# Kernel optimization log

Measured on AMD Instinct MI355X. Metric: run time of the kernel, lower is better.

## Reference

```python
import jax, jax.numpy as jnp
import numpy as np

EPS = 1e-5  # torch LayerNorm default


def setup_inputs() -> dict:
    key = jax.random.key(0)
    ks = jax.random.split(key, 4)
    N, E, D_IN, D_OUT = 10000, 640000, 128, 128
    x = jax.random.normal(ks[0], (N, D_IN), dtype=jnp.float32)
    edge_index = jax.random.randint(ks[1], (2, E), 0, N, dtype=jnp.int64)
    edge_weight = jax.random.uniform(ks[2], (E,), dtype=jnp.float32)
    W = jax.random.normal(ks[3], (D_IN, D_OUT), dtype=jnp.float32) / np.sqrt(D_IN)
    b = jnp.zeros((D_OUT,), dtype=jnp.float32)
    gamma = jnp.ones((D_OUT,), dtype=jnp.float32)
    beta = jnp.zeros((D_OUT,), dtype=jnp.float32)
    return {"x": x, "edge_index": edge_index, "edge_weight": edge_weight,
            "W": W, "b": b, "gamma": gamma, "beta": beta}


def reference(x, edge_index, edge_weight, W, b, gamma, beta):
    N = x.shape[0]
    src, dst = edge_index[0], edge_index[1]
    # in-degree (scatter_add of ones onto dst)
    deg = jax.ops.segment_sum(jnp.ones(dst.shape[0], dtype=x.dtype), dst,
                              num_segments=N)
    deg_inv = (deg + 1.0) ** -0.5  # [N]
    # gather-scale: per-edge messages [E, D]
    msgs = x[src] * deg_inv[src][:, None] * edge_weight[:, None]
    # scatter-add aggregation back to nodes [N, D]
    agg = jax.ops.segment_sum(msgs, dst, num_segments=N)
    agg = agg * deg_inv[:, None] + x  # symmetric norm + residual
    # linear + exact gelu (torch default) ; dropout is identity at eval
    h = jax.nn.gelu(agg @ W + b, approximate=False)
    # LayerNorm over last dim
    mu = jnp.mean(h, axis=-1, keepdims=True)
    var = jnp.mean((h - mu) ** 2, axis=-1, keepdims=True)
    return (h - mu) * jax.lax.rsqrt(var + EPS) * gamma + beta
```

## Files before the change

### kernel.cpp

```cpp
#include <hip/hip_runtime.h>
#include <math.h>


#define D 128
#define NB 512
#define NBK 256
#define MAXCHUNK 2560
#define MAXB 1600
#define FPSCALE 2097152.0f
#define FPINV (1.0f / 2097152.0f)

typedef short bf16x8 __attribute__((ext_vector_type(8)));
typedef float f32x4 __attribute__((ext_vector_type(4)));

static __device__ __forceinline__ unsigned bf16bits(float v) {
    unsigned u = __float_as_uint(v);
    return (u + 0x7fffu + ((u >> 16) & 1u)) >> 16;
}
static __device__ __forceinline__ int bkt_of(int d, unsigned N) {
    return (int)(((unsigned)d * NB) / N);
}
static __device__ __forceinline__ int bkt_start(int b, unsigned N) {
    return (int)(((unsigned)b * N + NB - 1) / NB);
}

__global__ __launch_bounds__(1024) void k_scatter(const int* __restrict__ srcIdx,
                                                  const int* __restrict__ dstIdx,
                                                  const float* __restrict__ ew,
                                                  uint2* __restrict__ tmp,
                                                  int* __restrict__ rp,
                                                  int E, int chunk, unsigned N) {
    __shared__ int hist[NB];
    __shared__ int scn[NB];
    __shared__ int cur[NB];
    __shared__ int dsts[MAXCHUNK];
    __shared__ uint2 sbuf[MAXCHUNK];
    int t = threadIdx.x, bb = blockIdx.x;
    int e0 = bb * chunk;
    int e1 = e0 + chunk; if (e1 > E) e1 = E;
    int n_loc = e1 - e0; if (n_loc < 0) n_loc = 0;
    for (int i = t; i < NB; i += 1024) hist[i] = 0;
    __syncthreads();
    for (int i = t; i < n_loc; i += 1024) {
        int d = dstIdx[e0 + i];
        dsts[i] = d;
        atomicAdd(&hist[bkt_of(d, N)], 1);
    }
    __syncthreads();
    if (t < NB) scn[t] = hist[t];
    __syncthreads();
    for (int o = 1; o < NB; o <<= 1) {
        int v = 0;
        if (t < NB && t >= o) v = scn[t - o];
        __syncthreads();
        if (t < NB && t >= o) scn[t] += v;
        __syncthreads();
    }
    if (t < NB) {
        int excl = scn[t] - hist[t];
        cur[t] = excl;
        rp[bb * (NB + 1) + t] = excl;
    }
    if (t == 0) rp[bb * (NB + 1) + NB] = n_loc;
    __syncthreads();
    for (int i = t; i < n_loc; i += 1024) {
        int d = dsts[i];
        int bin = bkt_of(d, N);
        int dl = d - bkt_start(bin, N);
        int pos = atomicAdd(&cur[bin], 1);
        sbuf[pos] = make_uint2((unsigned)srcIdx[e0 + i] | ((unsigned)dl << 16),
                               __float_as_uint(ew[e0 + i]));
    }
    __syncthreads();
    for (int i = t; i < n_loc; i += 1024)
        tmp[e0 + i] = sbuf[i];
}

__global__ __launch_bounds__(256) void k_xsdeg(const float* __restrict__ x,
                                               const uint2* __restrict__ tmp,
                                               const int* __restrict__ rp,
                                               unsigned* __restrict__ xs,
                                               int chunk, unsigned N) {
    __shared__ int segoff[NBK];
    __shared__ int segsrc[NBK];
    __shared__ int h[24];
    __shared__ float dinv[24];
    int b = blockIdx.x, t = threadIdx.x;
    int start = bkt_start(b, N), end = bkt_start(b + 1, N);
    int nn = end - start;
    if (t < NBK) {
        int lo = rp[t * (NB + 1) + b];
        int hi = rp[t * (NB + 1) + b + 1];
        segoff[t] = hi - lo;
        segsrc[t] = t * chunk + lo;
    }
    if (t < 24) h[t] = 0;
    __syncthreads();
    for (int o = 1; o < NBK; o <<= 1) {
        int v = 0;
        if (t < NBK && t >= o) v = segoff[t - o];
        __syncthreads();
        if (t < NBK && t >= o) segoff[t] += v;
        __syncthreads();
    }
    int cnt = segoff[NBK - 1];
    for (int i = t; i < cnt; i += 256) {
        int lo2 = 0, hi2 = NBK - 1;
        while (lo2 < hi2) { int mid = (lo2 + hi2) >> 1; if (segoff[mid] > i) hi2 = mid; else lo2 = mid + 1; }
        int base = lo2 ? segoff[lo2 - 1] : 0;
        uint2 rec = tmp[segsrc[lo2] + (i - base)];
        atomicAdd(&h[rec.x >> 16], 1);
    }
    __syncthreads();
    if (t < nn) dinv[t] = rsqrtf((float)h[t] + 1.0f);
    __syncthreads();
    for (int i = t; i < nn * 64; i += 256) {
        int nl = i >> 6, l = i & 63;
        int node = start + nl;
        float s = dinv[nl];
        float f0 = x[node * D + l] * s;
        float f1 = x[node * D + 64 + l] * s;
        xs[node * 64 + l] = bf16bits(f0) | (bf16bits(f1) << 16);
    }
}

__global__ __launch_bounds__(512) void k_mega(
    const float* __restrict__ x, const unsigned* __restrict__ xs,
    const uint2* __restrict__ tmp, const int* __restrict__ rp,
    const float* __restrict__ W, const float* __restrict__ bias,
    const float* __restrict__ gamma, const float* __restrict__ beta,
    float* __restrict__ out, int chunk, unsigned N) {
    __shared__ unsigned short wb[16384];
    __shared__ int segoff[NBK];
    __shared__ int segsrc[NBK];
    __shared__ uint2 reg1[MAXB];
    __shared__ unsigned reg2[2176];
    __shared__ int acc[20 * 128];
    __shared__ int h[24], st[24], cur[24];
    __shared__ float dinvs[24];
    __shared__ float bias_s[128], gamma_s[128], beta_s[128];
    __shared__ float s1s[4][2], s2s[4][2];

    float* hls = (float*)reg1;
    unsigned short* absb = (unsigned short*)reg2;
    unsigned* fin = reg2;

    int b = blockIdx.x, t = threadIdx.x;
    int start = bkt_start(b, N), end = bkt_start(b + 1, N);
    int nn = end - start;
    int wv = t >> 6, l = t & 63;

    for (int idx = t; idx < D * D; idx += 512) {
        int k = idx >> 7, n = idx & 127;
        wb[((k >> 3) * 128 + n) * 8 + (k & 7)] = (unsigned short)bf16bits(W[idx]);
    }
    if (t < 128) { bias_s[t] = bias[t]; gamma_s[t] = gamma[t]; beta_s[t] = beta[t]; }
    if (t < 24) h[t] = 0;

    if (t < NBK) {
        int lo = rp[t * (NB + 1) + b];
        int hi = rp[t * (NB + 1) + b + 1];
        segoff[t] = hi - lo;
        segsrc[t] = t * chunk + lo;
    }
    __syncthreads();
    for (int o = 1; o < NBK; o <<= 1) {
        int v = 0;
        if (t < NBK && t >= o) v = segoff[t - o];
        __syncthreads();
        if (t < NBK && t >= o) segoff[t] += v;
        __syncthreads();
    }
    int cnt = segoff[NBK - 1];
    int cntc = cnt > MAXB ? MAXB : cnt;

    for (int i = t; i < cntc; i += 512) {
        int lo2 = 0, hi2 = NBK - 1;
        while (lo2 < hi2) { int mid = (lo2 + hi2) >> 1; if (segoff[mid] > i) hi2 = mid; else lo2 = mid + 1; }
        int base = lo2 ? segoff[lo2 - 1] : 0;
        uint2 rec = tmp[segsrc[lo2] + (i - base)];
        reg1[i] = rec;
        atomicAdd(&h[rec.x >> 16], 1);
    }
    for (int i = t; i < 20 * 128; i += 512) acc[i] = 0;
    __syncthreads();

    if (t == 0) {
        st[0] = 0;
        for (int d2 = 0; d2 < nn; ++d2) st[d2 + 1] = st[d2] + h[d2];
    }
    if (t < nn) dinvs[t] = rsqrtf((float)h[t] + 1.0f);
    __syncthreads();
    if (t < nn) cur[t] = st[t];
    __syncthreads();

    for (int i = t; i < cntc; i += 512) {
        uint2 rec = reg1[i];
        int dl = (int)(rec.x >> 16);
        int pos = atomicAdd(&cur[dl], 1);
        fin[pos] = (rec.x & 0xffffu) | (bf16bits(__uint_as_float(rec.y)) << 16);
    }
    __syncthreads();

    {
        int lo = (int)(((long long)cntc * wv) >> 3);
        int hi = (int)(((long long)cntc * (wv + 1)) >> 3);
        if (lo < hi) {
            int dl = 0;
            while (st[dl + 1] <= lo) ++dl;
            float a0 = 0.0f, a1 = 0.0f;
            int i = lo;
            while (i < hi) {
                if (i >= st[dl + 1]) {
                    atomicAdd(&acc[dl * 128 + l], (int)(a0 * FPSCALE));
                    atomicAdd(&acc[dl * 128 + 64 + l], (int)(a1 * FPSCALE));
                    a0 = 0.0f; a1 = 0.0f;
                    do { ++dl; } while (i >= st[dl + 1]);
                }
                int stop = st[dl + 1] < hi ? st[dl + 1] : hi;
                for (; i + 4 <= stop; i += 4) {
                    unsigned p0 = fin[i], p1 = fin[i + 1], p2 = fin[i + 2], p3 = fin[i + 3];
                    unsigned q0 = xs[(p0 & 0xffffu) * 64u + (unsigned)l];
                    unsigned q1 = xs[(p1 & 0xffffu) * 64u + (unsigned)l];
                    unsigned q2 = xs[(p2 & 0xffffu) * 64u + (unsigned)l];
                    unsigned q3 = xs[(p3 & 0xffffu) * 64u + (unsigned)l];
                    float w0 = __uint_as_float(p0 & 0xffff0000u);
                    float w1 = __uint_as_float(p1 & 0xffff0000u);
                    float w2 = __uint_as_float(p2 & 0xffff0000u);
                    float w3 = __uint_as_float(p3 & 0xffff0000u);
                    a0 = fmaf(__uint_as_float(q0 << 16), w0, a0);
                    a1 = fmaf(__uint_as_float(q0 & 0xffff0000u), w0, a1);
                    a0 = fmaf(__uint_as_float(q1 << 16), w1, a0);
                    a1 = fmaf(__uint_as_float(q1 & 0xffff0000u), w1, a1);
                    a0 = fmaf(__uint_as_float(q2 << 16), w2, a0);
                    a1 = fmaf(__uint_as_float(q2 & 0xffff0000u), w2, a1);
                    a0 = fmaf(__uint_as_float(q3 << 16), w3, a0);
                    a1 = fmaf(__uint_as_float(q3 & 0xffff0000u), w3, a1);
                }
                for (; i < stop; ++i) {
                    unsigned p = fin[i];
                    float wt = __uint_as_float(p & 0xffff0000u);
                    unsigned q = xs[(p & 0xffffu) * 64u + (unsigned)l];
                    a0 = fmaf(__uint_as_float(q << 16), wt, a0);
                    a1 = fmaf(__uint_as_float(q & 0xffff0000u), wt, a1);
                }
            }
            atomicAdd(&acc[dl * 128 + l], (int)(a0 * FPSCALE));
            atomicAdd(&acc[dl * 128 + 64 + l], (int)(a1 * FPSCALE));
        }
    }
    __syncthreads();

    for (int i = t; i < 32 * 128; i += 512) {
        int row = i >> 7, col = i & 127;
        unsigned short v = 0;
        if (row < nn) {
            float aggv = (float)acc[row * 128 + col] * FPINV * dinvs[row]
                         + x[(start + row) * D + col];
            v = (unsigned short)bf16bits(aggv);
        }
        absb[row * 136 + col] = v;
    }
    __syncthreads();

    {
        int col = l & 15, quad = l >> 4;
#pragma unroll
        for (int ti = 0; ti < 2; ++ti) {
            int tid = wv * 2 + ti;
            int mt = tid >> 3, nt = tid & 7;
            f32x4 dacc = {0.0f, 0.0f, 0.0f, 0.0f};
#pragma unroll
            for (int kk = 0; kk < 4; ++kk) {
                bf16x8 av = *(const bf16x8*)&absb[(mt * 16 + col) * 136 + kk * 32 + quad * 8];
                bf16x8 bv = *(const bf16x8*)&wb[((kk * 4 + quad) * 128 + nt * 16 + col) * 8];
                dacc = __builtin_amdgcn_mfma_f32_16x16x32_bf16(av, bv, dacc, 0, 0, 0);
            }
#pragma unroll
            for (int r = 0; r < 4; ++r) {
                int m = mt * 16 + quad * 4 + r;
                int n = nt * 16 + col;
                if (m < 20) {
                    float hh = dacc[r] + bias_s[n];
                    hh = 0.5f * hh * (1.0f + erff(hh * 0.70710678f));
                    hls[m * 129 + n] = hh;
                }
            }
        }
    }
    __syncthreads();

    {
        int g = t >> 7;
        int tt = t & 127;
        int w2 = (t >> 6) & 1;
        for (int r = 0; r < 5; ++r) {
            int dl = r * 4 + g;
            bool valid = dl < nn;
            float hh = valid ? hls[dl * 129 + tt] : 0.0f;
            float v1 = hh, v2 = hh * hh;
#pragma unroll
            for (int o = 32; o > 0; o >>= 1) {
                v1 += __shfl_xor(v1, o, 64);
                v2 += __shfl_xor(v2, o, 64);
            }
            if (l == 0) { s1s[g][w2] = v1; s2s[g][w2] = v2; }
            __syncthreads();
            float s1 = s1s[g][0] + s1s[g][1];
            float s2 = s2s[g][0] + s2s[g][1];
            float mu = s1 * (1.0f / D);
            float var = s2 * (1.0f / D) - mu * mu;
            float rinv = rsqrtf(var + 1e-5f);
            if (valid)
                out[(start + dl) * D + tt] = (hh - mu) * rinv * gamma_s[tt] + beta_s[tt];
            __syncthreads();
        }
    }
}

static inline size_t align256(size_t v) { return (v + 255) & ~(size_t)255; }

extern "C" void kernel_launch(void* const* d_in, const int* in_sizes, int n_in,
                              void* d_out, int out_size, void* d_ws, size_t ws_size,
                              hipStream_t stream) {
    const float* x     = (const float*)d_in[0];
    const int*   ei    = (const int*)d_in[1];
    const float* ew    = (const float*)d_in[2];
    const float* W     = (const float*)d_in[3];
    const float* b     = (const float*)d_in[4];
    const float* gamma = (const float*)d_in[5];
    const float* beta  = (const float*)d_in[6];
    float* out = (float*)d_out;

    const int E = in_sizes[2];
    const unsigned N = (unsigned)(in_sizes[0] / D);
    const int chunk = (E + NBK - 1) / NBK;
    const int* srcIdx = ei;
    const int* dstIdx = ei + E;

    char* ws = (char*)d_ws;
    size_t off = 0;
    uint2* tmp = (uint2*)(ws + off);        off += align256((size_t)E * 8);
    int* rp = (int*)(ws + off);             off += align256((size_t)NBK * (NB + 1) * 4);
    unsigned* xs = (unsigned*)(ws + off);   off += align256((size_t)N * 64 * 4);
    (void)ws_size; (void)n_in; (void)out_size;

    k_scatter<<<NBK, 1024, 0, stream>>>(srcIdx, dstIdx, ew, tmp, rp, E, chunk, N);
    k_xsdeg<<<NB, 256, 0, stream>>>(x, tmp, rp, xs, chunk, N);
    k_mega<<<NB, 512, 0, stream>>>(x, xs, tmp, rp, W, b, gamma, beta, out, chunk, N);
}
```

Before: 119.1 us.

## Build per-bucket CSR once in k_build and reuse it in k_mega

Before, the per-bucket edge gather, histogram, prefix sum and counting sort ran twice: once in the degree kernel and again in the mega kernel. Now k_build does this work once and writes the compacted edge list and row starts to global workspace. k_mega just loads them, which removes the segment scan and binary-search gather from it and recomputes dinv from the row starts. It also overlays shared buffers to reduce LDS use and widens the gather unroll from 4 to 8 for more memory-level parallelism. The cost is an extra global write and read of the compacted edge list, plus more work in k_build.

```diff
diff --git a/kernel.cpp b/kernel.cpp
--- a/kernel.cpp
+++ b/kernel.cpp
@@ -76,14 +76,18 @@
         tmp[e0 + i] = sbuf[i];
 }
 
-__global__ __launch_bounds__(256) void k_xsdeg(const float* __restrict__ x,
+__global__ __launch_bounds__(256) void k_build(const float* __restrict__ x,
                                                const uint2* __restrict__ tmp,
                                                const int* __restrict__ rp,
+                                               unsigned* __restrict__ fin_g,
+                                               int* __restrict__ stg,
                                                unsigned* __restrict__ xs,
                                                int chunk, unsigned N) {
     __shared__ int segoff[NBK];
     __shared__ int segsrc[NBK];
-    __shared__ int h[24];
+    __shared__ uint2 buf[MAXB];
+    __shared__ unsigned finL[MAXB];
+    __shared__ int h[24], st[24], cur[24];
     __shared__ float dinv[24];
     int b = blockIdx.x, t = threadIdx.x;
     int start = bkt_start(b, N), end = bkt_start(b + 1, N);
@@ -104,16 +108,34 @@
         __syncthreads();
     }
     int cnt = segoff[NBK - 1];
-    for (int i = t; i < cnt; i += 256) {
+    int cntc = cnt > MAXB ? MAXB : cnt;
+    for (int i = t; i < cntc; i += 256) {
         int lo2 = 0, hi2 = NBK - 1;
         while (lo2 < hi2) { int mid = (lo2 + hi2) >> 1; if (segoff[mid] > i) hi2 = mid; else lo2 = mid + 1; }
         int base = lo2 ? segoff[lo2 - 1] : 0;
         uint2 rec = tmp[segsrc[lo2] + (i - base)];
+        buf[i] = rec;
         atomicAdd(&h[rec.x >> 16], 1);
     }
     __syncthreads();
+    if (t == 0) {
+        st[0] = 0;
+        for (int d2 = 0; d2 < nn; ++d2) st[d2 + 1] = st[d2] + h[d2];
+    }
     if (t < nn) dinv[t] = rsqrtf((float)h[t] + 1.0f);
     __syncthreads();
+    if (t < nn) cur[t] = st[t];
+    __syncthreads();
+    for (int i = t; i < cntc; i += 256) {
+        uint2 rec = buf[i];
+        int dl = (int)(rec.x >> 16);
+        int pos = atomicAdd(&cur[dl], 1);
+        finL[pos] = (rec.x & 0xffffu) | (bf16bits(__uint_as_float(rec.y)) << 16);
+    }
+    __syncthreads();
+    for (int i = t; i < cntc; i += 256)
+        fin_g[b * MAXB + i] = finL[i];
+    if (t <= nn) stg[b * 32 + t] = st[t];
     for (int i = t; i < nn * 64; i += 256) {
         int nl = i >> 6, l = i & 63;
         int node = start + nl;
@@ -126,24 +148,21 @@
 
 __global__ __launch_bounds__(512) void k_mega(
     const float* __restrict__ x, const unsigned* __restrict__ xs,
-    const uint2* __restrict__ tmp, const int* __restrict__ rp,
+    const unsigned* __restrict__ fin_g, const int* __restrict__ stg,
     const float* __restrict__ W, const float* __restrict__ bias,
     const float* __restrict__ gamma, const float* __restrict__ beta,
-    float* __restrict__ out, int chunk, unsigned N) {
+    float* __restrict__ out, unsigned N) {
     __shared__ unsigned short wb[16384];
-    __shared__ int segoff[NBK];
-    __shared__ int segsrc[NBK];
-    __shared__ uint2 reg1[MAXB];
-    __shared__ unsigned reg2[2176];
-    __shared__ int acc[20 * 128];
-    __shared__ int h[24], st[24], cur[24];
-    __shared__ float dinvs[24];
+    __shared__ __align__(16) char regA[8704];
+    __shared__ __align__(16) char regB[10320];
+    __shared__ int st[24];
     __shared__ float bias_s[128], gamma_s[128], beta_s[128];
     __shared__ float s1s[4][2], s2s[4][2];
 
-    float* hls = (float*)reg1;
-    unsigned short* absb = (unsigned short*)reg2;
-    unsigned* fin = reg2;
+    unsigned* finL = (unsigned*)regA;
+    unsigned short* absb = (unsigned short*)regA;
+    int* acc = (int*)regB;
+    float* hls = (float*)regB;
 
     int b = blockIdx.x, t = threadIdx.x;
     int start = bkt_start(b, N), end = bkt_start(b + 1, N);
@@ -155,51 +174,11 @@
         wb[((k >> 3) * 128 + n) * 8 + (k & 7)] = (unsigned short)bf16bits(W[idx]);
     }
     if (t < 128) { bias_s[t] = bias[t]; gamma_s[t] = gamma[t]; beta_s[t] = beta[t]; }
-    if (t < 24) h[t] = 0;
-
-    if (t < NBK) {
-        int lo = rp[t * (NB + 1) + b];
-        int hi = rp[t * (NB + 1) + b + 1];
-        segoff[t] = hi - lo;
-        segsrc[t] = t * chunk + lo;
-    }
-    __syncthreads();
-    for (int o = 1; o < NBK; o <<= 1) {
-        int v = 0;
-        if (t < NBK && t >= o) v = segoff[t - o];
-        __syncthreads();
-        if (t < NBK && t >= o) segoff[t] += v;
-        __syncthreads();
-    }
-    int cnt = segoff[NBK - 1];
-    int cntc = cnt > MAXB ? MAXB : cnt;
-
-    for (int i = t; i < cntc; i += 512) {
-        int lo2 = 0, hi2 = NBK - 1;
-        while (lo2 < hi2) { int mid = (lo2 + hi2) >> 1; if (segoff[mid] > i) hi2 = mid; else lo2 = mid + 1; }
-        int base = lo2 ? segoff[lo2 - 1] : 0;
-        uint2 rec = tmp[segsrc[lo2] + (i - base)];
-        reg1[i] = rec;
-        atomicAdd(&h[rec.x >> 16], 1);
-    }
+    if (t <= nn) st[t] = stg[b * 32 + t];
     for (int i = t; i < 20 * 128; i += 512) acc[i] = 0;
     __syncthreads();
-
-    if (t == 0) {
-        st[0] = 0;
-        for (int d2 = 0; d2 < nn; ++d2) st[d2 + 1] = st[d2] + h[d2];
-    }
-    if (t < nn) dinvs[t] = rsqrtf((float)h[t] + 1.0f);
-    __syncthreads();
-    if (t < nn) cur[t] = st[t];
-    __syncthreads();
-
-    for (int i = t; i < cntc; i += 512) {
-        uint2 rec = reg1[i];
-        int dl = (int)(rec.x >> 16);
-        int pos = atomicAdd(&cur[dl], 1);
-        fin[pos] = (rec.x & 0xffffu) | (bf16bits(__uint_as_float(rec.y)) << 16);
-    }
+    int cntc = st[nn];
+    for (int i = t; i < cntc; i += 512) finL[i] = fin_g[b * MAXB + i];
     __syncthreads();
 
     {
@@ -218,27 +197,21 @@
                     do { ++dl; } while (i >= st[dl + 1]);
                 }
                 int stop = st[dl + 1] < hi ? st[dl + 1] : hi;
-                for (; i + 4 <= stop; i += 4) {
-                    unsigned p0 = fin[i], p1 = fin[i + 1], p2 = fin[i + 2], p3 = fin[i + 3];
-                    unsigned q0 = xs[(p0 & 0xffffu) * 64u + (unsigned)l];
-                    unsigned q1 = xs[(p1 & 0xffffu) * 64u + (unsigned)l];
-                    unsigned q2 = xs[(p2 & 0xffffu) * 64u + (unsigned)l];
-                    unsigned q3 = xs[(p3 & 0xffffu) * 64u + (unsigned)l];
-                    float w0 = __uint_as_float(p0 & 0xffff0000u);
-                    float w1 = __uint_as_float(p1 & 0xffff0000u);
-                    float w2 = __uint_as_float(p2 & 0xffff0000u);
-                    float w3 = __uint_as_float(p3 & 0xffff0000u);
-                    a0 = fmaf(__uint_as_float(q0 << 16), w0, a0);
-                    a1 = fmaf(__uint_as_float(q0 & 0xffff0000u), w0, a1);
-                    a0 = fmaf(__uint_as_float(q1 << 16), w1, a0);
-                    a1 = fmaf(__uint_as_float(q1 & 0xffff0000u), w1, a1);
-                    a0 = fmaf(__uint_as_float(q2 << 16), w2, a0);
-                    a1 = fmaf(__uint_as_float(q2 & 0xffff0000u), w2, a1);
-                    a0 = fmaf(__uint_as_float(q3 << 16), w3, a0);
-                    a1 = fmaf(__uint_as_float(q3 & 0xffff0000u), w3, a1);
+                for (; i + 8 <= stop; i += 8) {
+                    unsigned p[8], q[8];
+#pragma unroll
+                    for (int j = 0; j < 8; ++j) p[j] = finL[i + j];
+#pragma unroll
+                    for (int j = 0; j < 8; ++j) q[j] = xs[(p[j] & 0xffffu) * 64u + (unsigned)l];
+#pragma unroll
+                    for (int j = 0; j < 8; ++j) {
+                        float wt = __uint_as_float(p[j] & 0xffff0000u);
+                        a0 = fmaf(__uint_as_float(q[j] << 16), wt, a0);
+                        a1 = fmaf(__uint_as_float(q[j] & 0xffff0000u), wt, a1);
+                    }
                 }
                 for (; i < stop; ++i) {
-                    unsigned p = fin[i];
+                    unsigned p = finL[i];
                     float wt = __uint_as_float(p & 0xffff0000u);
                     unsigned q = xs[(p & 0xffffu) * 64u + (unsigned)l];
                     a0 = fmaf(__uint_as_float(q << 16), wt, a0);
@@ -255,7 +228,8 @@
         int row = i >> 7, col = i & 127;
         unsigned short v = 0;
         if (row < nn) {
-            float aggv = (float)acc[row * 128 + col] * FPINV * dinvs[row]
+            float dv = rsqrtf((float)(st[row + 1] - st[row]) + 1.0f);
+            float aggv = (float)acc[row * 128 + col] * FPINV * dv
                          + x[(start + row) * D + col];
             v = (unsigned short)bf16bits(aggv);
         }
@@ -343,9 +317,11 @@
     uint2* tmp = (uint2*)(ws + off);        off += align256((size_t)E * 8);
     int* rp = (int*)(ws + off);             off += align256((size_t)NBK * (NB + 1) * 4);
     unsigned* xs = (unsigned*)(ws + off);   off += align256((size_t)N * 64 * 4);
+    unsigned* fin_g = (unsigned*)(ws + off); off += align256((size_t)NB * MAXB * 4);
+    int* stg = (int*)(ws + off);            off += align256((size_t)NB * 32 * 4);
     (void)ws_size; (void)n_in; (void)out_size;
 
     k_scatter<<<NBK, 1024, 0, stream>>>(srcIdx, dstIdx, ew, tmp, rp, E, chunk, N);
-    k_xsdeg<<<NB, 256, 0, stream>>>(x, tmp, rp, xs, chunk, N);
-    k_mega<<<NB, 512, 0, stream>>>(x, xs, tmp, rp, W, b, gamma, beta, out, chunk, N);
-}
+    k_build<<<NB, 256, 0, stream>>>(x, tmp, rp, fin_g, stg, xs, chunk, N);
+    k_mega<<<NB, 512, 0, stream>>>(x, xs, fin_g, stg, W, b, gamma, beta, out, N);
+}
```

Result: faster. 114.8 us (-3.6%).
